# Kernel optimization log

Hardware: AMD Instinct MI355X
Metric: run time of the kernel (lower is better)

## Reference

```python
import jax, jax.numpy as jnp
import numpy as np

B = 4096           # batch size
NG = 4096          # num_gene_sets (columns of input)
G = 1024           # number of aggregation groups
GS = 32            # members per group (CSR-packed; code handles ragged too)
T = G * GS         # total flat indices


def setup_inputs() -> dict:
    key = jax.random.key(0)
    k1, k2, k3 = jax.random.split(key, 3)
    gene_set_features = jax.random.normal(k1, (B, NG), dtype=jnp.float32)
    att_weights = jax.random.normal(k2, (T,), dtype=jnp.float32)  # concat of per-group logits
    flat_idx = jax.random.randint(k3, (T,), 0, NG, dtype=jnp.int64)
    segment_ids = (jnp.arange(T, dtype=jnp.int64) // GS)          # sorted group id per entry
    return {
        "gene_set_features": gene_set_features,
        "att_weights": att_weights,
        "flat_idx": flat_idx,
        "segment_ids": segment_ids,
        "num_segments": G,
    }


def reference(gene_set_features, att_weights, flat_idx, segment_ids, num_segments):
    # Per-group (segment) softmax over the batch-independent attention logits.
    seg_max = jax.ops.segment_max(att_weights, segment_ids, num_segments=num_segments)
    ex = jnp.exp(att_weights - seg_max[segment_ids])
    denom = jax.ops.segment_sum(ex, segment_ids, num_segments=num_segments)
    attn = ex / denom[segment_ids]                     # (T,) softmax weights per group
    # Gather all group members for every batch row in one shot, weight, segment-sum.
    gathered = gene_set_features[:, flat_idx]          # (B, T)
    weighted = gathered * attn[None, :]                # (B, T)
    out = jax.ops.segment_sum(weighted.T, segment_ids, num_segments=num_segments).T  # (B, G)
    return out
```

## Files before the change

### kernel.cpp

```cpp
#include <hip/hip_runtime.h>

#define NGK 4096
#define BK 4096
#define GK 1024
#define GSK 32
#define TK (GK * GSK)

#define BTILE 4
#define AGG_THREADS 256

__global__ __launch_bounds__(256) void seg_softmax_kernel(
        const float* __restrict__ att,
        const int*   __restrict__ idx,
        float2*      __restrict__ pairs) {
    int t = blockIdx.x * 256 + threadIdx.x;
    float w = att[t];

    float m = w;
    #pragma unroll
    for (int d = 16; d >= 1; d >>= 1) m = fmaxf(m, __shfl_xor(m, d, 32));
    float e = expf(w - m);
    float s = e;
    #pragma unroll
    for (int d = 16; d >= 1; d >>= 1) s += __shfl_xor(s, d, 32);

    pairs[t] = make_float2(e / s, __int_as_float(idx[t]));
}

__global__ __launch_bounds__(AGG_THREADS) void agg_kernel(
        const float*  __restrict__ F,
        const float2* __restrict__ pairs,
        float*        __restrict__ out) {
    __shared__ float lds[NGK * BTILE];

    const int tid = threadIdx.x;
    const long b0 = (long)blockIdx.x * BTILE;

    for (int p = tid; p < NGK * BTILE; p += AGG_THREADS) {
        int c = p >> 2;
        int r = p & 3;
        lds[p] = F[(b0 + r) * NGK + c];
    }
    __syncthreads();

    #pragma unroll
    for (int k = 0; k < GK / AGG_THREADS; ++k) {
        int g = tid + k * AGG_THREADS;
        float ax = 0.f, ay = 0.f, az = 0.f, aw = 0.f;
        const float2* pp = pairs + g * GSK;
        #pragma unroll 8
        for (int j = 0; j < GSK; ++j) {
            float2 pr = pp[j];
            float w = pr.x;
            int   c = __float_as_int(pr.y);
            const float4 v = *reinterpret_cast<const float4*>(&lds[c << 2]);
            ax += w * v.x;
            ay += w * v.y;
            az += w * v.z;
            aw += w * v.w;
        }
        out[(b0 + 0) * GK + g] = ax;
        out[(b0 + 1) * GK + g] = ay;
        out[(b0 + 2) * GK + g] = az;
        out[(b0 + 3) * GK + g] = aw;
    }
}

extern "C" void kernel_launch(void* const* d_in, const int* in_sizes, int n_in,
                              void* d_out, int out_size, void* d_ws, size_t ws_size,
                              hipStream_t stream) {
    const float* F   = (const float*)d_in[0];
    const float* att = (const float*)d_in[1];
    const int*   idx = (const int*)d_in[2];

    float2* pairs = (float2*)d_ws;
    float*  out   = (float*)d_out;

    seg_softmax_kernel<<<TK / 256, 256, 0, stream>>>(att, idx, pairs);
    agg_kernel<<<BK / BTILE, AGG_THREADS, 0, stream>>>(F, pairs, out);
}
```

Baseline: 137.8 us.

## Transpose softmax pairs for coalesced reads and vectorize LDS staging

The softmax kernel now writes the (weight, index) pairs transposed, group-minor, so that in the aggregation loop adjacent threads read adjacent pairs instead of each thread striding through its own 32-entry block. The LDS fill loads four batch rows per column and writes one float4, replacing four scalar LDS stores with strided global reads. Block size rises to 512 threads with a min-blocks hint of 4, so each thread handles two groups instead of four. The transposed scatter writes in the softmax kernel are uncoalesced, but that kernel is small.

```diff
diff --git a/kernel.cpp b/kernel.cpp
--- a/kernel.cpp
+++ b/kernel.cpp
@@ -7,12 +7,12 @@
 #define TK (GK * GSK)
 
 #define BTILE 4
-#define AGG_THREADS 256
+#define AGG_THREADS 512
 
 __global__ __launch_bounds__(256) void seg_softmax_kernel(
         const float* __restrict__ att,
         const int*   __restrict__ idx,
-        float2*      __restrict__ pairs) {
+        float2*      __restrict__ pairsT) {
     int t = blockIdx.x * 256 + threadIdx.x;
     float w = att[t];
 
@@ -24,22 +24,29 @@
     #pragma unroll
     for (int d = 16; d >= 1; d >>= 1) s += __shfl_xor(s, d, 32);
 
-    pairs[t] = make_float2(e / s, __int_as_float(idx[t]));
+    int g = t >> 5;
+    int j = t & 31;
+    pairsT[j * GK + g] = make_float2(e / s, __int_as_float(idx[t]));
 }
 
-__global__ __launch_bounds__(AGG_THREADS) void agg_kernel(
+__global__ __launch_bounds__(AGG_THREADS, 4) void agg_kernel(
         const float*  __restrict__ F,
-        const float2* __restrict__ pairs,
+        const float2* __restrict__ pairsT,
         float*        __restrict__ out) {
     __shared__ float lds[NGK * BTILE];
 
     const int tid = threadIdx.x;
-    const long b0 = (long)blockIdx.x * BTILE;
+    const int b0 = blockIdx.x * BTILE;
 
-    for (int p = tid; p < NGK * BTILE; p += AGG_THREADS) {
-        int c = p >> 2;
-        int r = p & 3;
-        lds[p] = F[(b0 + r) * NGK + c];
+    #pragma unroll
+    for (int it = 0; it < NGK / AGG_THREADS; ++it) {
+        int c = tid + it * AGG_THREADS;
+        float4 v;
+        v.x = F[(b0 + 0) * NGK + c];
+        v.y = F[(b0 + 1) * NGK + c];
+        v.z = F[(b0 + 2) * NGK + c];
+        v.w = F[(b0 + 3) * NGK + c];
+        *reinterpret_cast<float4*>(&lds[c << 2]) = v;
     }
     __syncthreads();
 
@@ -47,10 +54,9 @@
     for (int k = 0; k < GK / AGG_THREADS; ++k) {
         int g = tid + k * AGG_THREADS;
         float ax = 0.f, ay = 0.f, az = 0.f, aw = 0.f;
-        const float2* pp = pairs + g * GSK;
         #pragma unroll 8
         for (int j = 0; j < GSK; ++j) {
-            float2 pr = pp[j];
+            float2 pr = pairsT[j * GK + g];
             float w = pr.x;
             int   c = __float_as_int(pr.y);
             const float4 v = *reinterpret_cast<const float4*>(&lds[c << 2]);
@@ -73,9 +79,9 @@
     const float* att = (const float*)d_in[1];
     const int*   idx = (const int*)d_in[2];
 
-    float2* pairs = (float2*)d_ws;
-    float*  out   = (float*)d_out;
+    float2* pairsT = (float2*)d_ws;
+    float*  out    = (float*)d_out;
 
-    seg_softmax_kernel<<<TK / 256, 256, 0, stream>>>(att, idx, pairs);
-    agg_kernel<<<BK / BTILE, AGG_THREADS, 0, stream>>>(F, pairs, out);
+    seg_softmax_kernel<<<TK / 256, 256, 0, stream>>>(att, idx, pairsT);
+    agg_kernel<<<BK / BTILE, AGG_THREADS, 0, stream>>>(F, pairsT, out);
 }
```

Result: faster. 119.2 us (-13.5%).
